# Optimization experiments

Hardware: AMD Instinct MI355X
Metric: run time of the kernel (lower is better)

## Reference

```python
import jax, jax.numpy as jnp
import numpy as np

B, C_IN, C_MID, C_OUT, L = 32, 8, 128, 128, 512
T, DT = 50, 0.5
K = T // 2 + 1  # 26
DN = ('NCH', 'OIH', 'NCH')

def conv1d_same(x, w, b):
    # zero-padded 'SAME' Conv1d, kernel size 3
    y = jax.lax.conv_general_dilated(x, w, (1,), 'SAME', dimension_numbers=DN)
    return y + b[None, :, None]

def setup_inputs() -> dict:
    key = jax.random.key(0)
    ks = jax.random.split(key, 32)
    def n(k, shape, s=0.1):
        return jax.random.normal(k, shape, dtype=jnp.float32) * s
    inp = {}
    inp['x'] = jax.random.normal(ks[0], (B, C_IN, L), dtype=jnp.float32)
    # omega encoder (3 convs + ReLU)
    inp['ow1'] = n(ks[1], (C_MID, C_IN, 3));  inp['ob1'] = jnp.zeros((C_MID,), jnp.float32)
    inp['ow2'] = n(ks[2], (C_MID, C_MID, 3)); inp['ob2'] = jnp.zeros((C_MID,), jnp.float32)
    inp['ow3'] = n(ks[3], (C_OUT, C_MID, 3)); inp['ob3'] = jnp.zeros((C_OUT,), jnp.float32)
    # alpha encoder
    inp['aw1'] = n(ks[4], (C_MID, C_IN, 3));  inp['ab1'] = jnp.zeros((C_MID,), jnp.float32)
    inp['aw2'] = n(ks[5], (C_MID, C_MID, 3)); inp['ab2'] = jnp.zeros((C_MID,), jnp.float32)
    inp['aw3'] = n(ks[6], (C_OUT, C_MID, 3)); inp['ab3'] = jnp.zeros((C_OUT,), jnp.float32)
    # hy encoder (4 convs, last Tanh)
    inp['hw1'] = n(ks[7], (C_MID, C_IN, 3));  inp['hb1'] = jnp.zeros((C_MID,), jnp.float32)
    inp['hw2'] = n(ks[8], (C_MID, C_MID, 3)); inp['hb2'] = jnp.zeros((C_MID,), jnp.float32)
    inp['hw3'] = n(ks[9], (C_MID, C_MID, 3)); inp['hb3'] = jnp.zeros((C_MID,), jnp.float32)
    inp['hw4'] = n(ks[10], (C_OUT, C_MID, 3)); inp['hb4'] = jnp.zeros((C_OUT,), jnp.float32)
    # cell circular conv weight (no bias)
    inp['wy'] = n(ks[11], (C_OUT, C_OUT, 3))
    # linear readout
    inp['fct'] = n(ks[12], (K, T))                     # fc_time: T -> K, no bias
    inp['rw1'] = n(ks[13], (64, K * C_OUT)); inp['rb1'] = jnp.zeros((64,), jnp.float32)
    inp['rw2'] = n(ks[14], (32, 64));        inp['rb2'] = jnp.zeros((32,), jnp.float32)
    inp['rw3'] = n(ks[15], (1, 32));         inp['rb3'] = jnp.zeros((1,), jnp.float32)
    return inp

def reference(x, ow1, ob1, ow2, ob2, ow3, ob3,
              aw1, ab1, aw2, ab2, aw3, ab3,
              hw1, hb1, hw2, hb2, hw3, hb3, hw4, hb4,
              wy, fct, rw1, rb1, rw2, rb2, rw3, rb3):
    relu = jax.nn.relu
    omega = relu(conv1d_same(relu(conv1d_same(relu(conv1d_same(x, ow1, ob1)), ow2, ob2)), ow3, ob3))
    alpha = relu(conv1d_same(relu(conv1d_same(relu(conv1d_same(x, aw1, ab1)), aw2, ab2)), aw3, ab3))
    h = relu(conv1d_same(x, hw1, hb1))
    h = relu(conv1d_same(h, hw2, hb2))
    h = relu(conv1d_same(h, hw3, hb3))
    hy0 = jnp.tanh(conv1d_same(h, hw4, hb4))          # (B, C_OUT, L)
    hz0 = jnp.zeros_like(hy0)

    def circ_conv(h):
        # circular padding of 1 on each side, then VALID conv (matches padding_mode='circular')
        hp = jnp.concatenate([h[..., -1:], h, h[..., :1]], axis=-1)
        return jax.lax.conv_general_dilated(hp, wy, (1,), 'VALID', dimension_numbers=DN)

    def step(carry, _):
        hy, hz = carry
        spring = jnp.tanh(circ_conv(hy))
        hz = hz + DT * (spring - omega * hy - alpha * hz)
        hy = hy + DT * hz
        return (hy, hz), hy

    (_, _), ys = jax.lax.scan(step, (hy0, hz0), None, length=T)
    y_seq = jnp.transpose(ys, (1, 0, 2, 3))           # (B, T, C_OUT, L)

    # linear readout: fc_time over T, mean over L, MLP
    fft = jnp.einsum('btcl,kt->bkcl', y_seq, fct)     # (B, K, C_OUT, L)
    feat = fft.reshape(B, K * C_OUT, L).mean(axis=2)  # (B, K*C_OUT)
    h1 = relu(feat @ rw1.T + rb1)
    h2 = relu(h1 @ rw2.T + rb2)
    logits = h2 @ rw3.T + rb3                         # (B, 1)
    return logits, y_seq
```

## Files before the change

kernel.cpp:

```cpp
#include <hip/hip_runtime.h>
#include <math.h>

#define YB (50*128*512)
#define YT (128*512)
#define DTc 0.5f

typedef __attribute__((ext_vector_type(8))) short bf16x8;
typedef __attribute__((ext_vector_type(4))) float f32x4;

__device__ __forceinline__ unsigned short f2bf(float f) {
    unsigned int u = __builtin_bit_cast(unsigned int, f);
    u += 0x7fffu + ((u >> 16) & 1u);
    return (unsigned short)(u >> 16);
}

__device__ __forceinline__ float tanh_fast(float x) {
    float ax = fabsf(x);
    float e  = __expf(-2.f * ax);
    float r  = (1.f - e) * __builtin_amdgcn_rcpf(1.f + e);
    return __builtin_copysignf(r, x);
}

__device__ __forceinline__ void lds_sync() {
    asm volatile("s_waitcnt lgkmcnt(0)" ::: "memory");
    __builtin_amdgcn_sched_barrier(0);
    __builtin_amdgcn_s_barrier();
    __builtin_amdgcn_sched_barrier(0);
}

struct WSrc { const float* p[11]; };
__global__ void wprep_all_k(WSrc s, float* __restrict__ wt) {
    int idx = blockIdx.x * 256 + threadIdx.x;
    if (idx < 9216) {
        int wsel = idx / 3072, r = idx % 3072;
        int row = r >> 7, co = r & 127;
        int ci = row / 3, k = row - ci * 3;
        wt[idx] = s.p[wsel][(co * 8 + ci) * 3 + k];
    } else if (idx < 205824) {
        int r = idx - 9216;
        int wsel = 3 + r / 49152, q = r % 49152;
        int row = q >> 7, co = q & 127;
        int ci = row / 3, k = row - ci * 3;
        wt[idx] = s.p[wsel][(co * 128 + ci) * 3 + k];
    } else if (idx < 402432) {
        int q = idx - 205824;
        int cv = q / 49152, r = q % 49152;
        int co = r / 384, kap = r % 384;
        int k = kap >> 7;
        int ci = ((kap >> 5) & 3) * 32 + (kap & 31);
        int sel = (cv == 0) ? 10 : 6 + cv;
        ((unsigned short*)(wt + 205824))[q] = f2bf(s.p[sel][(co * 128 + ci) * 3 + k]);
    }
}

struct Job { const float* src; float* dst; const float* wt; const float* bias; int sbs, dbs, act; };
struct Jobs3 { Job j[3]; };

__global__ __launch_bounds__(256) void conv8x3_k(Jobs3 js) {
    int jb = blockIdx.y % 3;
    Job jo = js.j[jb];
    int b = blockIdx.z, tile = blockIdx.x, tid = threadIdx.x;
    int l0 = tile * 64;
    int tl4 = (tid & 15) * 4;
    int co0 = (tid >> 4) * 8;
    __shared__ float xs[8 * 68];
    __shared__ float wsh[24 * 128];
    const float* sb = jo.src + (size_t)b * jo.sbs;
    for (int idx = tid; idx < 8 * 66; idx += 256) {
        int ci = idx / 66, ll = idx - ci * 66;
        int gl = l0 - 1 + ll;
        xs[ci * 68 + ll] = (gl >= 0 && gl < 512) ? sb[ci * 512 + gl] : 0.f;
    }
    for (int idx = tid; idx < 24 * 128; idx += 256) wsh[idx] = jo.wt[idx];
    __syncthreads();
    float acc[8][4] = {};
    #pragma unroll
    for (int ci = 0; ci < 8; ++ci) {
        float x6[6];
        #pragma unroll
        for (int j = 0; j < 6; ++j) x6[j] = xs[ci * 68 + tl4 + j];
        #pragma unroll
        for (int k = 0; k < 3; ++k) {
            float w8[8];
            #pragma unroll
            for (int i = 0; i < 8; ++i) w8[i] = wsh[(ci * 3 + k) * 128 + co0 + i];
            #pragma unroll
            for (int i = 0; i < 8; ++i)
                #pragma unroll
                for (int j = 0; j < 4; ++j)
                    acc[i][j] = fmaf(w8[i], x6[k + j], acc[i][j]);
        }
    }
    #pragma unroll
    for (int i = 0; i < 8; ++i) {
        int co = co0 + i;
        float bv = jo.bias[co];
        float4 o;
        o.x = fmaxf(acc[i][0] + bv, 0.f);
        o.y = fmaxf(acc[i][1] + bv, 0.f);
        o.z = fmaxf(acc[i][2] + bv, 0.f);
        o.w = fmaxf(acc[i][3] + bv, 0.f);
        *(float4*)(jo.dst + (size_t)b * jo.dbs + (size_t)co * 512 + l0 + tl4) = o;
    }
}

__global__ __launch_bounds__(256) void conv128x3_k(Jobs3 js) {
    int jb = blockIdx.y >> 1, cb = blockIdx.y & 1;
    Job jo = js.j[jb];
    int b = blockIdx.z, tile = blockIdx.x, tid = threadIdx.x;
    int l0 = tile * 64;
    int tl4 = (tid & 15) * 4;
    int col = (tid >> 4) * 4;
    __shared__ float xs[32 * 68];
    __shared__ float wsh[96 * 64];
    const float* sb = jo.src + (size_t)b * jo.sbs;
    float acc[4][4] = {};
    for (int chunk = 0; chunk < 4; ++chunk) {
        for (int idx = tid; idx < 32 * 66; idx += 256) {
            int ci = idx / 66, ll = idx - ci * 66;
            int gl = l0 - 1 + ll;
            xs[ci * 68 + ll] = (gl >= 0 && gl < 512) ? sb[(chunk * 32 + ci) * 512 + gl] : 0.f;
        }
        for (int idx = tid; idx < 96 * 16; idx += 256) {
            int row = idx >> 4, j = (idx & 15) * 4;
            *(float4*)(wsh + row * 64 + j) =
                *(const float4*)(jo.wt + (size_t)(chunk * 96 + row) * 128 + cb * 64 + j);
        }
        __syncthreads();
        #pragma unroll 4
        for (int ci = 0; ci < 32; ++ci) {
            float x6[6];
            #pragma unroll
            for (int j = 0; j < 6; ++j) x6[j] = xs[ci * 68 + tl4 + j];
            #pragma unroll
            for (int k = 0; k < 3; ++k) {
                float w4[4];
                #pragma unroll
                for (int i = 0; i < 4; ++i) w4[i] = wsh[(ci * 3 + k) * 64 + col + i];
                #pragma unroll
                for (int i = 0; i < 4; ++i)
                    #pragma unroll
                    for (int j = 0; j < 4; ++j)
                        acc[i][j] = fmaf(w4[i], x6[k + j], acc[i][j]);
            }
        }
        __syncthreads();
    }
    #pragma unroll
    for (int i = 0; i < 4; ++i) {
        int co = cb * 64 + col + i;
        float bv = jo.bias[co];
        float v[4];
        #pragma unroll
        for (int j = 0; j < 4; ++j) {
            float tv = acc[i][j] + bv;
            if (jo.act == 1) tv = fmaxf(tv, 0.f);
            else if (jo.act == 2) tv = tanhf(tv);
            v[j] = tv;
        }
        *(float4*)(jo.dst + (size_t)b * jo.dbs + (size_t)co * 512 + l0 + tl4) = *(float4*)v;
    }
}

__global__ __launch_bounds__(512) void mconv_k(
    const float* __restrict__ src, int sbs,
    float* __restrict__ dst, int dbs,
    const unsigned short* __restrict__ w2,
    const float* __restrict__ bias, int act)
{
    int tile = blockIdx.x, b = blockIdx.y;
    int tid = threadIdx.x, lane = tid & 63, wid = tid >> 6;
    int lr = lane & 15, kg = lane >> 4;
    int co = wid * 16 + lr;
    int l0 = tile * 32;

    __shared__ float stage[128 * 40];
    __shared__ uint4 hyX[34 * 16];

    bf16x8 Bw[12];
    {
        const bf16x8* wp = (const bf16x8*)(w2 + (size_t)co * 384);
        #pragma unroll
        for (int s = 0; s < 12; ++s) Bw[s] = wp[s * 4 + kg];
    }

    const float* sb = src + (size_t)b * sbs;
    for (int i = tid; i < 1280; i += 512) {
        int c = i / 10, p4 = (i - c * 10) * 4;
        int l = l0 - 4 + p4;
        f32x4 v;
        if (l >= 0 && l <= 508) {
            v = *(const f32x4*)(sb + (size_t)c * 512 + l);
        } else {
            #pragma unroll
            for (int e = 0; e < 4; ++e) {
                int le = l + e;
                v[e] = (le >= 0 && le < 512) ? sb[(size_t)c * 512 + le] : 0.f;
            }
        }
        *(f32x4*)(stage + c * 40 + p4) = v;
    }
    __syncthreads();
    for (int i = tid; i < 34 * 16; i += 512) {
        int h = i >> 4, c8 = i & 15;
        unsigned short pk[8];
        #pragma unroll
        for (int q = 0; q < 8; ++q) pk[q] = f2bf(stage[(c8 * 8 + q) * 40 + h + 3]);
        hyX[h * 16 + (c8 ^ (h & 7))] = *(uint4*)pk;
    }
    __syncthreads();

    f32x4 acc[2];
    acc[0] = (f32x4){0.f, 0.f, 0.f, 0.f};
    acc[1] = (f32x4){0.f, 0.f, 0.f, 0.f};
    __builtin_amdgcn_s_setprio(1);
    #pragma unroll
    for (int s = 0; s < 12; ++s) {
        int k = s >> 2;
        int chunk = (s & 3) * 4 + kg;
        bf16x8 Bf = Bw[s];
        #pragma unroll
        for (int lt = 0; lt < 2; ++lt) {
            int arow = 16 * lt + lr + k;
            bf16x8 a = __builtin_bit_cast(bf16x8, hyX[arow * 16 + ((arow & 7) ^ chunk)]);
            acc[lt] = __builtin_amdgcn_mfma_f32_16x16x32_bf16(a, Bf, acc[lt], 0, 0, 0);
        }
    }
    __builtin_amdgcn_s_setprio(0);

    float bv = bias[co];
    #pragma unroll
    for (int lt = 0; lt < 2; ++lt) {
        float v[4];
        #pragma unroll
        for (int j = 0; j < 4; ++j) {
            float t = acc[lt][j] + bv;
            v[j] = (act == 1) ? fmaxf(t, 0.f) : tanh_fast(t);
        }
        *(f32x4*)(dst + (size_t)b * dbs + (size_t)co * 512 + l0 + 16 * lt + 4 * kg) = *(f32x4*)v;
    }
}

__global__ __launch_bounds__(512, 2) void chunk_k(
    const float* __restrict__ hy_in,
    const float* __restrict__ hz_in,
    float* __restrict__ hz_out,
    const float* __restrict__ omega, const float* __restrict__ alpha,
    const unsigned short* __restrict__ w2,
    float* __restrict__ ybase,
    float* __restrict__ part, int t0, int ns)
{
    int tile = blockIdx.x, b = blockIdx.y;
    int tid = threadIdx.x, lane = tid & 63, wid = tid >> 6;
    int lr = lane & 15, kg = lane >> 4;
    int co = wid * 16 + lr;
    int l0 = tile * 32;

    __shared__ uint4 hySd[2][800];
    __shared__ float ytmp[2 * 4608];
    float* stage = ytmp;

    bf16x8 Bw[12];
    {
        const bf16x8* wp = (const bf16x8*)(w2 + (size_t)co * 384);
        #pragma unroll
        for (int s = 0; s < 12; ++s) Bw[s] = wp[s * 4 + kg];
    }

    f32x4 hyR[3], hzR[3], omR[3], alR[3];

    {
        const float* src = hy_in + (size_t)b * YB;
        for (int i = tid; i < 128 * 14; i += 512) {
            int c = i / 14, p4 = (i - c * 14) * 4;
            int l = (l0 - 12 + p4) & 511;
            *(f32x4*)(stage + c * 56 + p4) = *(const f32x4*)(src + (size_t)c * 512 + l);
        }
    }
    __syncthreads();
    #pragma unroll
    for (int lt = 0; lt < 3; ++lt)
        hyR[lt] = *(const f32x4*)(stage + co * 56 + 16 * lt + 4 * kg + 4);
    for (int i = tid; i < 50 * 16; i += 512) {
        int h = i >> 4, c8 = i & 15;
        unsigned short pk[8];
        #pragma unroll
        for (int q = 0; q < 8; ++q) pk[q] = f2bf(stage[(c8 * 8 + q) * 56 + h + 3]);
        hySd[0][h * 16 + (c8 ^ (h & 7))] = *(uint4*)pk;
    }
    {
        size_t ob = (size_t)b * 65536 + (size_t)co * 512;
        #pragma unroll
        for (int lt = 0; lt < 3; ++lt) {
            int l = (l0 - 8 + 16 * lt + 4 * kg) & 511;
            omR[lt] = *(const f32x4*)(omega + ob + l);
            alR[lt] = *(const f32x4*)(alpha + ob + l);
            if (t0 > 0) hzR[lt] = *(const f32x4*)(hz_in + ob + l);
            else        hzR[lt] = (f32x4){0.f, 0.f, 0.f, 0.f};
        }
    }
    __syncthreads();

    for (int i = 0; i < ns; ++i) {
        const uint4* hc = &hySd[i & 1][0];
        unsigned short* hn16 = (unsigned short*)&hySd[(i + 1) & 1][0];
        float* yt = ytmp + (i & 1) * 4608;

        f32x4 acc[3];
        #pragma unroll
        for (int lt = 0; lt < 3; ++lt) acc[lt] = (f32x4){0.f, 0.f, 0.f, 0.f};
        __builtin_amdgcn_s_setprio(1);
        #pragma unroll
        for (int s = 0; s < 12; ++s) {
            int chunk = (s & 3) * 4 + kg;
            int k = s >> 2;
            bf16x8 Bf = Bw[s];
            #pragma unroll
            for (int lt = 0; lt < 3; ++lt) {
                int arow = 16 * lt + lr + k;
                bf16x8 a = __builtin_bit_cast(bf16x8, hc[arow * 16 + ((arow & 7) ^ chunk)]);
                acc[lt] = __builtin_amdgcn_mfma_f32_16x16x32_bf16(a, Bf, acc[lt], 0, 0, 0);
            }
        }
        __builtin_amdgcn_s_setprio(0);

        float lsum = 0.f;
        #pragma unroll
        for (int lt = 0; lt < 3; ++lt) {
            #pragma unroll
            for (int j = 0; j < 4; ++j) {
                float spring = tanh_fast(acc[lt][j]);
                float zn = hzR[lt][j] + DTc * (spring - omR[lt][j] * hyR[lt][j] - alR[lt][j] * hzR[lt][j]);
                float hn = hyR[lt][j] + DTc * zn;
                hzR[lt][j] = zn;
                hyR[lt][j] = hn;
            }
            bool valid = (lt == 0) ? (kg >= 2) : (lt == 2) ? (kg < 2) : true;
            int r0 = 16 * lt + 4 * kg;
            if (valid) {
                *(f32x4*)(yt + co * 36 + (r0 - 8)) = hyR[lt];
                lsum += hyR[lt][0] + hyR[lt][1] + hyR[lt][2] + hyR[lt][3];
                if (i == ns - 1)
                    *(f32x4*)(hz_out + (size_t)b * 65536 + (size_t)co * 512 + l0 + (r0 - 8)) = hzR[lt];
            }
            if (i < ns - 1) {
                #pragma unroll
                for (int j = 0; j < 4; ++j) {
                    int rr = r0 + j + 1;
                    int sidx = rr * 128 + (((co >> 3) ^ (rr & 7)) << 3) + (co & 7);
                    hn16[sidx] = f2bf(hyR[lt][j]);
                }
            }
        }
        lsum += __shfl_xor(lsum, 16);
        lsum += __shfl_xor(lsum, 32);
        if (kg == 0) part[(((size_t)b * 50 + t0 + i) * 128 + co) * 16 + tile] = lsum;

        lds_sync();

        {
            float* yrow = ybase + (size_t)b * YB + (size_t)i * YT;
            int cs = wid * 16 + (lane >> 3);
            int lq = (lane & 7) * 4;
            #pragma unroll
            for (int cq = 0; cq < 2; ++cq) {
                int c2 = cs + cq * 8;
                f32x4 v = *(const f32x4*)(yt + c2 * 36 + lq);
                *(f32x4*)(yrow + (size_t)c2 * 512 + l0 + lq) = v;
            }
        }
    }
}

__global__ __launch_bounds__(256) void readout_k(
    const float* __restrict__ part, const float* __restrict__ fct,
    const float* __restrict__ rw1, const float* __restrict__ rb1,
    const float* __restrict__ rw2, const float* __restrict__ rb2,
    const float* __restrict__ rw3, const float* __restrict__ rb3,
    float* __restrict__ out)
{
    int b = blockIdx.x, tid = threadIdx.x;
    __shared__ float ybar[50 * 128];
    __shared__ float feat[26 * 128];
    __shared__ float h1[64];
    __shared__ float h2[32];
    for (int idx = tid; idx < 50 * 128; idx += 256) {
        const float* p = part + ((size_t)b * 6400 + idx) * 16;
        float s = 0.f;
        #pragma unroll
        for (int q = 0; q < 16; ++q) s += p[q];
        ybar[idx] = s * (1.f / 512.f);
    }
    __syncthreads();
    for (int idx = tid; idx < 26 * 128; idx += 256) {
        int k = idx >> 7, c = idx & 127;
        float s = 0.f;
        for (int t = 0; t < 50; ++t) s += fct[k * 50 + t] * ybar[t * 128 + c];
        feat[idx] = s;
    }
    __syncthreads();
    {
        int j = tid >> 2, q = tid & 3;
        float s = 0.f;
        const float* r = rw1 + (size_t)j * 3328 + q * 832;
        const float* f = feat + q * 832;
        for (int i = 0; i < 832; ++i) s += f[i] * r[i];
        s += __shfl_xor(s, 1);
        s += __shfl_xor(s, 2);
        if (q == 0) h1[j] = fmaxf(s + rb1[j], 0.f);
    }
    __syncthreads();
    if (tid < 32) {
        float s = 0.f;
        for (int i = 0; i < 64; ++i) s += h1[i] * rw2[tid * 64 + i];
        h2[tid] = fmaxf(s + rb2[tid], 0.f);
    }
    __syncthreads();
    if (tid == 0) {
        float s = 0.f;
        for (int i = 0; i < 32; ++i) s += h2[i] * rw3[i];
        out[b] = s + rb3[0];
    }
}

extern "C" void kernel_launch(void* const* d_in, const int* in_sizes, int n_in,
                              void* d_out, int out_size, void* d_ws, size_t ws_size,
                              hipStream_t stream)
{
    const float* x   = (const float*)d_in[0];
    const float* ow1 = (const float*)d_in[1];  const float* ob1 = (const float*)d_in[2];
    const float* ow2 = (const float*)d_in[3];  const float* ob2 = (const float*)d_in[4];
    const float* ow3 = (const float*)d_in[5];  const float* ob3 = (const float*)d_in[6];
    const float* aw1 = (const float*)d_in[7];  const float* ab1 = (const float*)d_in[8];
    const float* aw2 = (const float*)d_in[9];  const float* ab2 = (const float*)d_in[10];
    const float* aw3 = (const float*)d_in[11]; const float* ab3 = (const float*)d_in[12];
    const float* hw1 = (const float*)d_in[13]; const float* hb1 = (const float*)d_in[14];
    const float* hw2 = (const float*)d_in[15]; const float* hb2 = (const float*)d_in[16];
    const float* hw3 = (const float*)d_in[17]; const float* hb3 = (const float*)d_in[18];
    const float* hw4 = (const float*)d_in[19]; const float* hb4 = (const float*)d_in[20];
    const float* wy  = (const float*)d_in[21];
    const float* fct = (const float*)d_in[22];
    const float* rw1 = (const float*)d_in[23]; const float* rb1 = (const float*)d_in[24];
    const float* rw2 = (const float*)d_in[25]; const float* rb2 = (const float*)d_in[26];
    const float* rw3 = (const float*)d_in[27]; const float* rb3 = (const float*)d_in[28];

    float* out  = (float*)d_out;
    float* yout = out + 32;
    float* ws   = (float*)d_ws;

    float* OMEGA = ws;
    float* ALPHA = ws + 2097152;
    float* WT    = ws + 4194304;
    float* PART  = ws + 4547584;
    float* HZ0   = ws + 7824384;
    float* HZ1   = ws + 9921536;

    float* To1 = yout + 44 * YT;
    float* Ta1 = yout + 45 * YT;
    float* Th1 = yout + 46 * YT;
    float* To2 = yout + 47 * YT;
    float* Ta2 = yout + 43 * YT;
    float* Th2 = yout + 49 * YT;
    float* Th3 = yout + 42 * YT;
    float* HY0 = yout + 48 * YT;

    float* OW1T = WT + 0;      float* AW1T = WT + 3072;   float* HW1T = WT + 6144;
    float* OW2T = WT + 9216;   float* OW3T = WT + 58368;
    float* AW2T = WT + 107520; float* AW3T = WT + 156672;
    unsigned short* W2WY = (unsigned short*)(WT + 205824);
    unsigned short* W2H2 = W2WY + 49152;
    unsigned short* W2H3 = W2WY + 98304;
    unsigned short* W2H4 = W2WY + 147456;

    WSrc wsrc;
    wsrc.p[0] = ow1; wsrc.p[1] = aw1; wsrc.p[2] = hw1;
    wsrc.p[3] = ow2; wsrc.p[4] = ow3; wsrc.p[5] = aw2; wsrc.p[6] = aw3;
    wsrc.p[7] = hw2; wsrc.p[8] = hw3; wsrc.p[9] = hw4; wsrc.p[10] = wy;
    wprep_all_k<<<1572, 256, 0, stream>>>(wsrc, WT);

    Jobs3 d1 = {{ {x, To1, OW1T, ob1, 4096, YB, 1},
                  {x, Ta1, AW1T, ab1, 4096, YB, 1},
                  {x, Th1, HW1T, hb1, 4096, YB, 1} }};
    conv8x3_k<<<dim3(8, 3, 32), 256, 0, stream>>>(d1);

    Jobs3 d2 = {{ {To1, To2, OW2T, ob2, YB, YB, 1},
                  {Ta1, Ta2, AW2T, ab2, YB, YB, 1},
                  {To1, To2, OW2T, ob2, YB, YB, 1} }};
    conv128x3_k<<<dim3(8, 4, 32), 256, 0, stream>>>(d2);

    Jobs3 d3 = {{ {To2, OMEGA, OW3T, ob3, YB, 65536, 1},
                  {Ta2, ALPHA, AW3T, ab3, YB, 65536, 1},
                  {To2, OMEGA, OW3T, ob3, YB, 65536, 1} }};
    conv128x3_k<<<dim3(8, 4, 32), 256, 0, stream>>>(d3);

    mconv_k<<<dim3(16, 32), 512, 0, stream>>>(Th1, YB, Th2, YB, W2H2, hb2, 1);
    mconv_k<<<dim3(16, 32), 512, 0, stream>>>(Th2, YB, Th3, YB, W2H3, hb3, 1);
    mconv_k<<<dim3(16, 32), 512, 0, stream>>>(Th3, YB, HY0, YB, W2H4, hb4, 2);

    {
        int t0 = 0, c = 0;
        while (t0 < 50) {
            int ns = (50 - t0 >= 8) ? 8 : (50 - t0);
            const float* hyin = (t0 == 0) ? HY0 : (yout + (size_t)(t0 - 1) * YT);
            const float* hzin = (c & 1) ? HZ1 : HZ0;
            float* hzout      = (c & 1) ? HZ0 : HZ1;
            chunk_k<<<dim3(16, 32), 512, 0, stream>>>(hyin, hzin, hzout,
                                                      OMEGA, ALPHA, W2WY,
                                                      yout + (size_t)t0 * YT, PART, t0, ns);
            t0 += ns; ++c;
        }
    }

    readout_k<<<32, 256, 0, stream>>>(PART, fct, rw1, rb1, rw2, rb2, rw3, rb3, out);
}
```

Before: 627.1 us.

## Move omega/alpha 128-channel convs to split-bf16 MFMA and pass bf16 hy between chunks

Replaces the scalar FP32 conv128x3 kernel for the omega and alpha encoders with an MFMA kernel. To keep near-fp32 accuracy it splits both activations and weights into bf16 hi and lo parts and issues three MFMAs per step (hi*hi, lo*hi, hi*lo). The recurrence chunk kernel now reads and writes a transposed bf16 hy tile through a ping-pong buffer, which removes the per-chunk fp32 staging and conversion pass. In exchange it costs extra weight prep, workspace and a little precision loss from dropping the lo*lo term.

```diff
diff --git a/kernel.cpp b/kernel.cpp
--- a/kernel.cpp
+++ b/kernel.cpp
@@ -12,6 +12,10 @@
     unsigned int u = __builtin_bit_cast(unsigned int, f);
     u += 0x7fffu + ((u >> 16) & 1u);
     return (unsigned short)(u >> 16);
+}
+__device__ __forceinline__ float bf2f(unsigned short h) {
+    unsigned int u = ((unsigned int)h) << 16;
+    return __builtin_bit_cast(float, u);
 }
 
 __device__ __forceinline__ float tanh_fast(float x) {
@@ -36,20 +40,17 @@
         int row = r >> 7, co = r & 127;
         int ci = row / 3, k = row - ci * 3;
         wt[idx] = s.p[wsel][(co * 8 + ci) * 3 + k];
-    } else if (idx < 205824) {
-        int r = idx - 9216;
-        int wsel = 3 + r / 49152, q = r % 49152;
-        int row = q >> 7, co = q & 127;
-        int ci = row / 3, k = row - ci * 3;
-        wt[idx] = s.p[wsel][(co * 128 + ci) * 3 + k];
-    } else if (idx < 402432) {
-        int q = idx - 205824;
+    } else if (idx < 9216 + 589824) {
+        int q = idx - 9216;
         int cv = q / 49152, r = q % 49152;
         int co = r / 384, kap = r % 384;
         int k = kap >> 7;
         int ci = ((kap >> 5) & 3) * 32 + (kap & 31);
-        int sel = (cv == 0) ? 10 : 6 + cv;
-        ((unsigned short*)(wt + 205824))[q] = f2bf(s.p[sel][(co * 128 + ci) * 3 + k]);
+        const int selmap[12] = {10, 7, 8, 9, 3, 3, 4, 4, 5, 5, 6, 6};
+        float w = s.p[selmap[cv]][(co * 128 + ci) * 3 + k];
+        unsigned short hv = f2bf(w);
+        unsigned short ov = ((cv >= 4) && (cv & 1)) ? f2bf(w - bf2f(hv)) : hv;
+        ((unsigned short*)(wt + 9216))[q] = ov;
     }
 }
 
@@ -104,69 +105,12 @@
     }
 }
 
-__global__ __launch_bounds__(256) void conv128x3_k(Jobs3 js) {
-    int jb = blockIdx.y >> 1, cb = blockIdx.y & 1;
-    Job jo = js.j[jb];
-    int b = blockIdx.z, tile = blockIdx.x, tid = threadIdx.x;
-    int l0 = tile * 64;
-    int tl4 = (tid & 15) * 4;
-    int col = (tid >> 4) * 4;
-    __shared__ float xs[32 * 68];
-    __shared__ float wsh[96 * 64];
-    const float* sb = jo.src + (size_t)b * jo.sbs;
-    float acc[4][4] = {};
-    for (int chunk = 0; chunk < 4; ++chunk) {
-        for (int idx = tid; idx < 32 * 66; idx += 256) {
-            int ci = idx / 66, ll = idx - ci * 66;
-            int gl = l0 - 1 + ll;
-            xs[ci * 68 + ll] = (gl >= 0 && gl < 512) ? sb[(chunk * 32 + ci) * 512 + gl] : 0.f;
-        }
-        for (int idx = tid; idx < 96 * 16; idx += 256) {
-            int row = idx >> 4, j = (idx & 15) * 4;
-            *(float4*)(wsh + row * 64 + j) =
-                *(const float4*)(jo.wt + (size_t)(chunk * 96 + row) * 128 + cb * 64 + j);
-        }
-        __syncthreads();
-        #pragma unroll 4
-        for (int ci = 0; ci < 32; ++ci) {
-            float x6[6];
-            #pragma unroll
-            for (int j = 0; j < 6; ++j) x6[j] = xs[ci * 68 + tl4 + j];
-            #pragma unroll
-            for (int k = 0; k < 3; ++k) {
-                float w4[4];
-                #pragma unroll
-                for (int i = 0; i < 4; ++i) w4[i] = wsh[(ci * 3 + k) * 64 + col + i];
-                #pragma unroll
-                for (int i = 0; i < 4; ++i)
-                    #pragma unroll
-                    for (int j = 0; j < 4; ++j)
-                        acc[i][j] = fmaf(w4[i], x6[k + j], acc[i][j]);
-            }
-        }
-        __syncthreads();
-    }
-    #pragma unroll
-    for (int i = 0; i < 4; ++i) {
-        int co = cb * 64 + col + i;
-        float bv = jo.bias[co];
-        float v[4];
-        #pragma unroll
-        for (int j = 0; j < 4; ++j) {
-            float tv = acc[i][j] + bv;
-            if (jo.act == 1) tv = fmaxf(tv, 0.f);
-            else if (jo.act == 2) tv = tanhf(tv);
-            v[j] = tv;
-        }
-        *(float4*)(jo.dst + (size_t)b * jo.dbs + (size_t)co * 512 + l0 + tl4) = *(float4*)v;
-    }
-}
-
 __global__ __launch_bounds__(512) void mconv_k(
     const float* __restrict__ src, int sbs,
     float* __restrict__ dst, int dbs,
     const unsigned short* __restrict__ w2,
-    const float* __restrict__ bias, int act)
+    const float* __restrict__ bias, int act,
+    unsigned short* __restrict__ hyt)
 {
     int tile = blockIdx.x, b = blockIdx.y;
     int tid = threadIdx.x, lane = tid & 63, wid = tid >> 6;
@@ -229,19 +173,124 @@
     __builtin_amdgcn_s_setprio(0);
 
     float bv = bias[co];
+    float vv[2][4];
+    #pragma unroll
+    for (int lt = 0; lt < 2; ++lt) {
+        #pragma unroll
+        for (int j = 0; j < 4; ++j) {
+            float t = acc[lt][j] + bv;
+            vv[lt][j] = (act == 1) ? fmaxf(t, 0.f) : tanh_fast(t);
+        }
+        *(f32x4*)(dst + (size_t)b * dbs + (size_t)co * 512 + l0 + 16 * lt + 4 * kg) = *(f32x4*)vv[lt];
+    }
+
+    if (hyt) {
+        lds_sync();
+        unsigned short* t16 = (unsigned short*)hyX;
+        #pragma unroll
+        for (int lt = 0; lt < 2; ++lt)
+            #pragma unroll
+            for (int j = 0; j < 4; ++j)
+                t16[(16 * lt + 4 * kg + j) * 128 + co] = f2bf(vv[lt][j]);
+        lds_sync();
+        int row = tid >> 4, c8 = tid & 15;
+        ((uint4*)hyt)[((size_t)b * 512 + l0 + row) * 16 + c8] =
+            ((uint4*)hyX)[row * 16 + c8];
+    }
+}
+
+struct MJob { const float* src; float* dst; const unsigned short* whi;
+              const unsigned short* wlo; const float* bias; int sbs, dbs; };
+struct MJobs2 { MJob j[2]; };
+
+__global__ __launch_bounds__(512) void mconv2_k(MJobs2 js) {
+    MJob jo = js.j[blockIdx.z];
+    int tile = blockIdx.x, b = blockIdx.y;
+    int tid = threadIdx.x, lane = tid & 63, wid = tid >> 6;
+    int lr = lane & 15, kg = lane >> 4;
+    int co = wid * 16 + lr;
+    int l0 = tile * 32;
+
+    __shared__ float stage[128 * 40];
+    __shared__ uint4 hiX[34 * 16];
+    __shared__ uint4 loX[34 * 16];
+
+    const bf16x8* wph = (const bf16x8*)(jo.whi + (size_t)co * 384);
+    const bf16x8* wpl = (const bf16x8*)(jo.wlo + (size_t)co * 384);
+    bf16x8 Bh[12];
+    #pragma unroll
+    for (int s = 0; s < 12; ++s) Bh[s] = wph[s * 4 + kg];
+
+    const float* sb = jo.src + (size_t)b * jo.sbs;
+    for (int i = tid; i < 1280; i += 512) {
+        int c = i / 10, p4 = (i - c * 10) * 4;
+        int l = l0 - 4 + p4;
+        f32x4 v;
+        if (l >= 0 && l <= 508) {
+            v = *(const f32x4*)(sb + (size_t)c * 512 + l);
+        } else {
+            #pragma unroll
+            for (int e = 0; e < 4; ++e) {
+                int le = l + e;
+                v[e] = (le >= 0 && le < 512) ? sb[(size_t)c * 512 + le] : 0.f;
+            }
+        }
+        *(f32x4*)(stage + c * 40 + p4) = v;
+    }
+    __syncthreads();
+    for (int i = tid; i < 34 * 16; i += 512) {
+        int h = i >> 4, c8 = i & 15;
+        unsigned short ph[8], pl[8];
+        #pragma unroll
+        for (int q = 0; q < 8; ++q) {
+            float x = stage[(c8 * 8 + q) * 40 + h + 3];
+            unsigned short hv = f2bf(x);
+            ph[q] = hv;
+            pl[q] = f2bf(x - bf2f(hv));
+        }
+        int sx = h * 16 + (c8 ^ (h & 7));
+        hiX[sx] = *(uint4*)ph;
+        loX[sx] = *(uint4*)pl;
+    }
+    __syncthreads();
+
+    f32x4 acc[2];
+    acc[0] = (f32x4){0.f, 0.f, 0.f, 0.f};
+    acc[1] = (f32x4){0.f, 0.f, 0.f, 0.f};
+    bf16x8 blc = wpl[kg];
+    __builtin_amdgcn_s_setprio(1);
+    #pragma unroll
+    for (int s = 0; s < 12; ++s) {
+        bf16x8 Bl = blc;
+        if (s < 11) blc = wpl[(s + 1) * 4 + kg];
+        int k = s >> 2;
+        int chunk = (s & 3) * 4 + kg;
+        #pragma unroll
+        for (int lt = 0; lt < 2; ++lt) {
+            int arow = 16 * lt + lr + k;
+            int ai = arow * 16 + ((arow & 7) ^ chunk);
+            bf16x8 ah = __builtin_bit_cast(bf16x8, hiX[ai]);
+            bf16x8 al = __builtin_bit_cast(bf16x8, loX[ai]);
+            acc[lt] = __builtin_amdgcn_mfma_f32_16x16x32_bf16(ah, Bh[s], acc[lt], 0, 0, 0);
+            acc[lt] = __builtin_amdgcn_mfma_f32_16x16x32_bf16(al, Bh[s], acc[lt], 0, 0, 0);
+            acc[lt] = __builtin_amdgcn_mfma_f32_16x16x32_bf16(ah, Bl,    acc[lt], 0, 0, 0);
+        }
+    }
+    __builtin_amdgcn_s_setprio(0);
+
+    float bv = jo.bias[co];
     #pragma unroll
     for (int lt = 0; lt < 2; ++lt) {
         float v[4];
         #pragma unroll
-        for (int j = 0; j < 4; ++j) {
-            float t = acc[lt][j] + bv;
-            v[j] = (act == 1) ? fmaxf(t, 0.f) : tanh_fast(t);
-        }
-        *(f32x4*)(dst + (size_t)b * dbs + (size_t)co * 512 + l0 + 16 * lt + 4 * kg) = *(f32x4*)v;
+        for (int j = 0; j < 4; ++j) v[j] = fmaxf(acc[lt][j] + bv, 0.f);
+        *(f32x4*)(jo.dst + (size_t)b * jo.dbs + (size_t)co * 512 + l0 + 16 * lt + 4 * kg) = *(f32x4*)v;
     }
 }
 
 __global__ __launch_bounds__(512, 2) void chunk_k(
+    const unsigned short* __restrict__ hyt_in,
+    unsigned short* __restrict__ hyt_out,
     const float* __restrict__ hy_in,
     const float* __restrict__ hz_in,
     float* __restrict__ hz_out,
@@ -258,7 +307,6 @@
 
     __shared__ uint4 hySd[2][800];
     __shared__ float ytmp[2 * 4608];
-    float* stage = ytmp;
 
     bf16x8 Bw[12];
     {
@@ -270,29 +318,20 @@
     f32x4 hyR[3], hzR[3], omR[3], alR[3];
 
     {
+        const uint4* hsrc = (const uint4*)hyt_in + (size_t)b * 8192;
+        for (int i = tid; i < 800; i += 512) {
+            int h = i >> 4, c8 = i & 15;
+            int l = (l0 - 9 + h) & 511;
+            hySd[0][h * 16 + (c8 ^ (h & 7))] = hsrc[l * 16 + c8];
+        }
+    }
+    {
         const float* src = hy_in + (size_t)b * YB;
-        for (int i = tid; i < 128 * 14; i += 512) {
-            int c = i / 14, p4 = (i - c * 14) * 4;
-            int l = (l0 - 12 + p4) & 511;
-            *(f32x4*)(stage + c * 56 + p4) = *(const f32x4*)(src + (size_t)c * 512 + l);
-        }
-    }
-    __syncthreads();
-    #pragma unroll
-    for (int lt = 0; lt < 3; ++lt)
-        hyR[lt] = *(const f32x4*)(stage + co * 56 + 16 * lt + 4 * kg + 4);
-    for (int i = tid; i < 50 * 16; i += 512) {
-        int h = i >> 4, c8 = i & 15;
-        unsigned short pk[8];
-        #pragma unroll
-        for (int q = 0; q < 8; ++q) pk[q] = f2bf(stage[(c8 * 8 + q) * 56 + h + 3]);
-        hySd[0][h * 16 + (c8 ^ (h & 7))] = *(uint4*)pk;
-    }
-    {
         size_t ob = (size_t)b * 65536 + (size_t)co * 512;
         #pragma unroll
         for (int lt = 0; lt < 3; ++lt) {
             int l = (l0 - 8 + 16 * lt + 4 * kg) & 511;
+            hyR[lt] = *(const f32x4*)(src + (size_t)co * 512 + l);
             omR[lt] = *(const f32x4*)(omega + ob + l);
             alR[lt] = *(const f32x4*)(alpha + ob + l);
             if (t0 > 0) hzR[lt] = *(const f32x4*)(hz_in + ob + l);
@@ -343,13 +382,11 @@
                 if (i == ns - 1)
                     *(f32x4*)(hz_out + (size_t)b * 65536 + (size_t)co * 512 + l0 + (r0 - 8)) = hzR[lt];
             }
-            if (i < ns - 1) {
-                #pragma unroll
-                for (int j = 0; j < 4; ++j) {
-                    int rr = r0 + j + 1;
-                    int sidx = rr * 128 + (((co >> 3) ^ (rr & 7)) << 3) + (co & 7);
-                    hn16[sidx] = f2bf(hyR[lt][j]);
-                }
+            #pragma unroll
+            for (int j = 0; j < 4; ++j) {
+                int rr = r0 + j + 1;
+                int sidx = rr * 128 + (((co >> 3) ^ (rr & 7)) << 3) + (co & 7);
+                hn16[sidx] = f2bf(hyR[lt][j]);
             }
         }
         lsum += __shfl_xor(lsum, 16);
@@ -369,6 +406,14 @@
                 *(f32x4*)(yrow + (size_t)c2 * 512 + l0 + lq) = v;
             }
         }
+    }
+
+    {
+        const uint4* hl = &hySd[ns & 1][0];
+        int row = tid >> 4, c8 = tid & 15;
+        int h = row + 9;
+        ((uint4*)hyt_out)[((size_t)b * 512 + l0 + row) * 16 + c8] =
+            hl[h * 16 + (c8 ^ (h & 7))];
     }
 }
 
@@ -451,9 +496,11 @@
     float* OMEGA = ws;
     float* ALPHA = ws + 2097152;
     float* WT    = ws + 4194304;
-    float* PART  = ws + 4547584;
-    float* HZ0   = ws + 7824384;
-    float* HZ1   = ws + 9921536;
+    float* PART  = ws + 4498432;
+    float* HZ0   = ws + 7775232;
+    float* HZ1   = ws + 9872384;
+    unsigned short* HYT0 = (unsigned short*)(ws + 11969536);
+    unsigned short* HYT1 = (unsigned short*)(ws + 13018112);
 
     float* To1 = yout + 44 * YT;
     float* Ta1 = yout + 45 * YT;
@@ -464,47 +511,49 @@
     float* Th3 = yout + 42 * YT;
     float* HY0 = yout + 48 * YT;
 
-    float* OW1T = WT + 0;      float* AW1T = WT + 3072;   float* HW1T = WT + 6144;
-    float* OW2T = WT + 9216;   float* OW3T = WT + 58368;
-    float* AW2T = WT + 107520; float* AW3T = WT + 156672;
-    unsigned short* W2WY = (unsigned short*)(WT + 205824);
-    unsigned short* W2H2 = W2WY + 49152;
-    unsigned short* W2H3 = W2WY + 98304;
-    unsigned short* W2H4 = W2WY + 147456;
+    float* OW1T = WT + 0;  float* AW1T = WT + 3072;  float* HW1T = WT + 6144;
+    unsigned short* U16 = (unsigned short*)(WT + 9216);
+    unsigned short* W2WY = U16;
+    unsigned short* W2H2 = U16 + 49152;
+    unsigned short* W2H3 = U16 + 98304;
+    unsigned short* W2H4 = U16 + 147456;
+    unsigned short* OW2H = U16 + 196608;  unsigned short* OW2L = U16 + 245760;
+    unsigned short* OW3H = U16 + 294912;  unsigned short* OW3L = U16 + 344064;
+    unsigned short* AW2H = U16 + 393216;  unsigned short* AW2L = U16 + 442368;
+    unsigned short* AW3H = U16 + 491520;  unsigned short* AW3L = U16 + 540672;
 
     WSrc wsrc;
     wsrc.p[0] = ow1; wsrc.p[1] = aw1; wsrc.p[2] = hw1;
     wsrc.p[3] = ow2; wsrc.p[4] = ow3; wsrc.p[5] = aw2; wsrc.p[6] = aw3;
     wsrc.p[7] = hw2; wsrc.p[8] = hw3; wsrc.p[9] = hw4; wsrc.p[10] = wy;
-    wprep_all_k<<<1572, 256, 0, stream>>>(wsrc, WT);
+    wprep_all_k<<<2340, 256, 0, stream>>>(wsrc, WT);
 
     Jobs3 d1 = {{ {x, To1, OW1T, ob1, 4096, YB, 1},
                   {x, Ta1, AW1T, ab1, 4096, YB, 1},
                   {x, Th1, HW1T, hb1, 4096, YB, 1} }};
     conv8x3_k<<<dim3(8, 3, 32), 256, 0, stream>>>(d1);
 
-    Jobs3 d2 = {{ {To1, To2, OW2T, ob2, YB, YB, 1},
-                  {Ta1, Ta2, AW2T, ab2, YB, YB, 1},
-                  {To1, To2, OW2T, ob2, YB, YB, 1} }};
-    conv128x3_k<<<dim3(8, 4, 32), 256, 0, stream>>>(d2);
-
-    Jobs3 d3 = {{ {To2, OMEGA, OW3T, ob3, YB, 65536, 1},
-                  {Ta2, ALPHA, AW3T, ab3, YB, 65536, 1},
-                  {To2, OMEGA, OW3T, ob3, YB, 65536, 1} }};
-    conv128x3_k<<<dim3(8, 4, 32), 256, 0, stream>>>(d3);
-
-    mconv_k<<<dim3(16, 32), 512, 0, stream>>>(Th1, YB, Th2, YB, W2H2, hb2, 1);
-    mconv_k<<<dim3(16, 32), 512, 0, stream>>>(Th2, YB, Th3, YB, W2H3, hb3, 1);
-    mconv_k<<<dim3(16, 32), 512, 0, stream>>>(Th3, YB, HY0, YB, W2H4, hb4, 2);
+    MJobs2 e2 = {{ {To1, To2, OW2H, OW2L, ob2, YB, YB},
+                   {Ta1, Ta2, AW2H, AW2L, ab2, YB, YB} }};
+    mconv2_k<<<dim3(16, 32, 2), 512, 0, stream>>>(e2);
+    MJobs2 e3 = {{ {To2, OMEGA, OW3H, OW3L, ob3, YB, 65536},
+                   {Ta2, ALPHA, AW3H, AW3L, ab3, YB, 65536} }};
+    mconv2_k<<<dim3(16, 32, 2), 512, 0, stream>>>(e3);
+
+    mconv_k<<<dim3(16, 32), 512, 0, stream>>>(Th1, YB, Th2, YB, W2H2, hb2, 1, nullptr);
+    mconv_k<<<dim3(16, 32), 512, 0, stream>>>(Th2, YB, Th3, YB, W2H3, hb3, 1, nullptr);
+    mconv_k<<<dim3(16, 32), 512, 0, stream>>>(Th3, YB, HY0, YB, W2H4, hb4, 2, HYT0);
 
     {
         int t0 = 0, c = 0;
         while (t0 < 50) {
             int ns = (50 - t0 >= 8) ? 8 : (50 - t0);
+            const unsigned short* hin = (c & 1) ? HYT1 : HYT0;
+            unsigned short* hout      = (c & 1) ? HYT0 : HYT1;
             const float* hyin = (t0 == 0) ? HY0 : (yout + (size_t)(t0 - 1) * YT);
             const float* hzin = (c & 1) ? HZ1 : HZ0;
             float* hzout      = (c & 1) ? HZ0 : HZ1;
-            chunk_k<<<dim3(16, 32), 512, 0, stream>>>(hyin, hzin, hzout,
+            chunk_k<<<dim3(16, 32), 512, 0, stream>>>(hin, hout, hyin, hzin, hzout,
                                                       OMEGA, ALPHA, W2WY,
                                                       yout + (size_t)t0 * YT, PART, t0, ns);
             t0 += ns; ++c;
```

New measurement: 546.2 us. 12.9% less time.
